# Kernel tuning notes

Hardware: AMD Instinct MI355X
Metric: run time of the kernel (lower is better)

The kernel has to match this reference:

```python
import jax, jax.numpy as jnp
import numpy as np

N = 100000   # nodes
E = 1600000  # edges (avg degree 16)
IN = 64
HID = 16     # hardcoded in ChebNet.conv1
OUT = 40
K = 3


def setup_inputs() -> dict:
    key = jax.random.key(0)
    k0, k1, k2, k3 = jax.random.split(key, 4)
    x = jax.random.normal(k0, (N, IN), jnp.float32)
    edge_index = jax.random.randint(k1, (2, E), 0, N, jnp.int32)
    # Glorot-style init for the K per-order linear maps of each ChebConv
    s1 = float(np.sqrt(2.0 / (IN + HID)))
    W1 = jax.random.normal(k2, (K, IN, HID), jnp.float32) * s1
    b1 = jnp.zeros((HID,), jnp.float32)
    s2 = float(np.sqrt(2.0 / (HID + OUT)))
    W2 = jax.random.normal(k3, (K, HID, OUT), jnp.float32) * s2
    b2 = jnp.zeros((OUT,), jnp.float32)
    return {"x": x, "edge_index": edge_index, "W1": W1, "b1": b1, "W2": W2, "b2": b2}


def cheb_conv(x, edge_index, W, b):
    """PyG ChebConv with normalization='sym', lambda_max=2.
    Scaled Laplacian: L_hat = 2L/lambda_max - I = -D^{-1/2} A D^{-1/2} (diag 0).
    out = sum_k T_k(L_hat) x @ W[k] + b, T0=x, T1=L_hat x, Tk=2 L_hat T_{k-1}-T_{k-2}.
    """
    row, col = edge_index[0], edge_index[1]
    ones = jnp.ones((edge_index.shape[1],), x.dtype)
    deg = jax.ops.segment_sum(ones, row, num_segments=N)
    dis = jnp.where(deg > 0, jax.lax.rsqrt(jnp.maximum(deg, 1.0)), 0.0)
    norm = -(dis[row] * dis[col])  # [E]

    def Lhat(z):  # sparse scatter-gather: gather src rows, scale, scatter-add to dst
        return jax.ops.segment_sum(norm[:, None] * z[row], col, num_segments=N)

    Tx0 = x
    out = Tx0 @ W[0]
    Tx1 = Lhat(x)
    if W.shape[0] > 1:
        out = out + Tx1 @ W[1]
    for k in range(2, W.shape[0]):
        Tx2 = 2.0 * Lhat(Tx1) - Tx0
        out = out + Tx2 @ W[k]
        Tx0, Tx1 = Tx1, Tx2
    return out + b


def reference(x, edge_index, W1, b1, W2, b2):
    h = jax.nn.relu(cheb_conv(x, edge_index, W1, b1))
    h = cheb_conv(h, edge_index, W2, b2)
    return jax.nn.log_softmax(h, axis=1)
```

## Files before the change

kernel.cpp:

```cpp
#include <hip/hip_runtime.h>
#include <hip/hip_bf16.h>


typedef unsigned short u16;

constexpr int N_    = 100000;
constexpr int E_    = 1600000;
constexpr int IN_   = 64;
constexpr int HID_  = 16;
constexpr int OUT_  = 40;
constexpr int CAP_  = 48;
constexpr int S_    = 64;
constexpr int EPS_  = E_ / S_;
constexpr int P8_   = 8;
constexpr int NPP8_ = N_ / P8_;
constexpr int P4_   = 4;
constexpr int NPP4_ = N_ / P4_;
constexpr int NPAD_ = 100352;

__device__ __forceinline__ float bf2f(u16 u) {
    return __uint_as_float((unsigned)u << 16);
}
__device__ __forceinline__ u16 f2bf(float x) {
    unsigned u = __float_as_uint(x);
    return (u16)((u + 0x7FFFu + ((u >> 16) & 1u)) >> 16);
}

__global__ void deg_part(const int* __restrict__ row, u16* __restrict__ partial) {
    __shared__ int lds[NPP8_];
    int p = blockIdx.x >> 6, s = blockIdx.x & 63;
    for (int i = threadIdx.x; i < NPP8_; i += 256) lds[i] = 0;
    __syncthreads();
    int lo = p * NPP8_, e0 = s * EPS_;
    for (int i = threadIdx.x; i < EPS_; i += 256) {
        int r = row[e0 + i];
        unsigned d = (unsigned)(r - lo);
        if (d < (unsigned)NPP8_) atomicAdd(&lds[d], 1);
    }
    __syncthreads();
    u16* dst = partial + (size_t)blockIdx.x * NPP8_;
    for (int i = threadIdx.x; i < NPP8_; i += 256) dst[i] = (u16)lds[i];
}

__global__ void __launch_bounds__(1024)
hist_in(const int* __restrict__ col, u16* __restrict__ partial) {
    __shared__ int lds[NPP4_];
    int p = blockIdx.x >> 6, s = blockIdx.x & 63;
    for (int i = threadIdx.x; i < NPP4_; i += 1024) lds[i] = 0;
    __syncthreads();
    int lo = p * NPP4_, e0 = s * EPS_;
    for (int i = threadIdx.x; i < EPS_; i += 1024) {
        int c = col[e0 + i];
        unsigned d = (unsigned)(c - lo);
        if (d < (unsigned)NPP4_) atomicAdd(&lds[d], 1);
    }
    __syncthreads();
    u16* dst = partial + (size_t)blockIdx.x * NPP4_;
    for (int i = threadIdx.x; i < NPP4_; i += 1024) dst[i] = (u16)lds[i];
}

__global__ void __launch_bounds__(1024)
reduce_all(const u16* __restrict__ partial_row, const u16* __restrict__ partial_in,
           float* __restrict__ dis, u16* __restrict__ pre, int* __restrict__ indeg) {
    int n = blockIdx.x * 1024 + threadIdx.x;
    if (n >= N_) return;
    {
        int p = n / NPP8_, i = n - p * NPP8_;
        const u16* base = partial_row + (size_t)(p * S_) * NPP8_ + i;
        int d = 0;
#pragma unroll 8
        for (int s = 0; s < S_; ++s) d += base[(size_t)s * NPP8_];
        dis[n] = (d > 0) ? rsqrtf((float)d) : 0.0f;
    }
    {
        int p = n / NPP4_, i = n - p * NPP4_;
        const u16* base = partial_in + (size_t)(p * S_) * NPP4_ + i;
        int run = 0;
#pragma unroll 8
        for (int s = 0; s < S_; ++s) {
            pre[(size_t)s * NPAD_ + n] = (u16)run;
            run += base[(size_t)s * NPP4_];
        }
        indeg[n] = run;
    }
}

__global__ void __launch_bounds__(1024)
place_proj(const int* __restrict__ row, const int* __restrict__ col,
           const float* __restrict__ x, const float* __restrict__ W,
           const float* __restrict__ dis, const u16* __restrict__ pre,
           int* __restrict__ bucket,
           float* __restrict__ P0f, float* __restrict__ P2f,
           u16* __restrict__ A1, u16* __restrict__ A2) {
    __shared__ int pos[NPP4_];
    __shared__ float w[3 * IN_ * HID_];
    if (blockIdx.x < 256) {
        int p = blockIdx.x >> 6, s = blockIdx.x & 63;
        int lo = p * NPP4_, e0 = s * EPS_;
        const u16* psrc = pre + (size_t)s * NPAD_ + lo;
        for (int i = threadIdx.x; i < NPP4_; i += 1024) pos[i] = psrc[i];
        __syncthreads();
        for (int i = threadIdx.x; i < EPS_; i += 1024) {
            int c = col[e0 + i];
            unsigned d = (unsigned)(c - lo);
            if (d < (unsigned)NPP4_) {
                int r = row[e0 + i];
                int q = atomicAdd(&pos[d], 1);
                if (q < CAP_) bucket[(size_t)c * CAP_ + q] = r;
            }
        }
    } else {
        for (int i = threadIdx.x; i < 3 * IN_ * HID_; i += 1024) w[i] = W[i];
        __syncthreads();
        int t = (blockIdx.x - 256) * 1024 + threadIdx.x;
        if (t >= N_ * HID_) return;
        int n = t >> 4, j = t & 15;
        const float* xr = x + (size_t)n * IN_;
        float a0 = 0.f, a1 = 0.f, a2 = 0.f;
#pragma unroll
        for (int i = 0; i < IN_; ++i) {
            float xv = xr[i];
            a0 += xv * w[i * 16 + j];
            a1 += xv * w[1024 + i * 16 + j];
            a2 += xv * w[2048 + i * 16 + j];
        }
        float dn = dis[n];
        P0f[t] = a0;
        P2f[t] = a2;
        A1[t] = f2bf(dn * a1);
        A2[t] = f2bf(dn * a2);
    }
}

__global__ void g32b(const u16* __restrict__ A1, const u16* __restrict__ A2,
                     const int* __restrict__ indeg, const int* __restrict__ bucket,
                     const float* __restrict__ dis,
                     float* __restrict__ LP1f, u16* __restrict__ B2) {
    int wib = threadIdx.x >> 6, lane = threadIdx.x & 63;
    int n0 = (blockIdx.x * 4 + wib) * 4;
    int eg = lane >> 3, sub = lane & 7;
    const u16* Z = (sub < 4) ? A1 : A2;
    int fq = sub & 3;
    int m[4];
#pragma unroll
    for (int k = 0; k < 4; ++k) m[k] = min(indeg[n0 + k], CAP_);
    float ax[4] = {0,0,0,0}, ay[4] = {0,0,0,0}, az[4] = {0,0,0,0}, aw[4] = {0,0,0,0};
#pragma unroll
    for (int k = 0; k < 4; ++k) {
        int n = n0 + k;
        for (int base = 0; base < m[k]; base += 8) {
            int e = base + eg;
            if (e < m[k]) {
                int r = bucket[n * CAP_ + e];
                ushort4 zv = *(const ushort4*)&Z[(size_t)r * 16 + fq * 4];
                ax[k] += bf2f(zv.x); ay[k] += bf2f(zv.y);
                az[k] += bf2f(zv.z); aw[k] += bf2f(zv.w);
            }
        }
    }
#pragma unroll
    for (int off = 8; off < 64; off <<= 1) {
#pragma unroll
        for (int k = 0; k < 4; ++k) {
            ax[k] += __shfl_xor(ax[k], off, 64); ay[k] += __shfl_xor(ay[k], off, 64);
            az[k] += __shfl_xor(az[k], off, 64); aw[k] += __shfl_xor(aw[k], off, 64);
        }
    }
    if (lane < 8) {
#pragma unroll
        for (int k = 0; k < 4; ++k) {
            int n = n0 + k;
            float dn = dis[n];
            if (lane < 4) {
                float4 v = {-dn * ax[k], -dn * ay[k], -dn * az[k], -dn * aw[k]};
                *(float4*)&LP1f[(size_t)n * 16 + fq * 4] = v;
            } else {
                float s = -(dn * dn);
                ushort4 v = {f2bf(s * ax[k]), f2bf(s * ay[k]),
                             f2bf(s * az[k]), f2bf(s * aw[k])};
                *(ushort4*)&B2[(size_t)n * 16 + fq * 4] = v;
            }
        }
    }
}

__device__ __forceinline__ void g16core4(const u16* __restrict__ Z,
                                         const int* __restrict__ indeg,
                                         const int* __restrict__ bucket,
                                         int n0, int lane, float4 acc[4]) {
    int eg = lane >> 2, fq = lane & 3;
    int m[4];
#pragma unroll
    for (int k = 0; k < 4; ++k) m[k] = min(indeg[n0 + k], CAP_);
    float ax[4] = {0,0,0,0}, ay[4] = {0,0,0,0}, az[4] = {0,0,0,0}, aw[4] = {0,0,0,0};
#pragma unroll
    for (int k = 0; k < 4; ++k) {
        int n = n0 + k;
        for (int base = 0; base < m[k]; base += 16) {
            int e = base + eg;
            if (e < m[k]) {
                int r = bucket[n * CAP_ + e];
                ushort4 zv = *(const ushort4*)&Z[(size_t)r * 16 + fq * 4];
                ax[k] += bf2f(zv.x); ay[k] += bf2f(zv.y);
                az[k] += bf2f(zv.z); aw[k] += bf2f(zv.w);
            }
        }
    }
#pragma unroll
    for (int off = 4; off < 64; off <<= 1) {
#pragma unroll
        for (int k = 0; k < 4; ++k) {
            ax[k] += __shfl_xor(ax[k], off, 64); ay[k] += __shfl_xor(ay[k], off, 64);
            az[k] += __shfl_xor(az[k], off, 64); aw[k] += __shfl_xor(aw[k], off, 64);
        }
    }
#pragma unroll
    for (int k = 0; k < 4; ++k) {
        float4 r4 = {ax[k], ay[k], az[k], aw[k]};
        acc[k] = r4;
    }
}

__global__ void g16_combine(const u16* __restrict__ B2, const int* __restrict__ indeg,
                            const int* __restrict__ bucket, const float* __restrict__ dis,
                            const float* __restrict__ LP1f, const float* __restrict__ P2f,
                            const float* __restrict__ b1,
                            float* p0h , u16* __restrict__ Hs) {
    int wib = threadIdx.x >> 6, lane = threadIdx.x & 63;
    int n0 = (blockIdx.x * 4 + wib) * 4;
    float4 acc[4];
    g16core4(B2, indeg, bucket, n0, lane, acc);
    if (lane < 4) {
#pragma unroll
        for (int k = 0; k < 4; ++k) {
            int n = n0 + k;
            float dn = dis[n];
            float4 p0 = *(const float4*)&p0h[(size_t)n * 16 + lane * 4];
            float4 lp = *(const float4*)&LP1f[(size_t)n * 16 + lane * 4];
            float4 p2 = *(const float4*)&P2f[(size_t)n * 16 + lane * 4];
            float4 bb = *(const float4*)&b1[lane * 4];
            float4 hv;
            hv.x = fmaxf(p0.x + lp.x - 2.f * dn * acc[k].x - p2.x + bb.x, 0.f);
            hv.y = fmaxf(p0.y + lp.y - 2.f * dn * acc[k].y - p2.y + bb.y, 0.f);
            hv.z = fmaxf(p0.z + lp.z - 2.f * dn * acc[k].z - p2.z + bb.z, 0.f);
            hv.w = fmaxf(p0.w + lp.w - 2.f * dn * acc[k].w - p2.w + bb.w, 0.f);
            *(float4*)&p0h[(size_t)n * 16 + lane * 4] = hv;
            ushort4 hs = {f2bf(dn * hv.x), f2bf(dn * hv.y),
                          f2bf(dn * hv.z), f2bf(dn * hv.w)};
            *(ushort4*)&Hs[(size_t)n * 16 + lane * 4] = hs;
        }
    }
}

__global__ void g16_t1(const u16* __restrict__ Hs, const int* __restrict__ indeg,
                       const int* __restrict__ bucket, const float* __restrict__ dis,
                       float* __restrict__ T1f, u16* __restrict__ Ts) {
    int wib = threadIdx.x >> 6, lane = threadIdx.x & 63;
    int n0 = (blockIdx.x * 4 + wib) * 4;
    float4 acc[4];
    g16core4(Hs, indeg, bucket, n0, lane, acc);
    if (lane < 4) {
#pragma unroll
        for (int k = 0; k < 4; ++k) {
            int n = n0 + k;
            float dn = dis[n];
            float4 t1 = {-dn * acc[k].x, -dn * acc[k].y, -dn * acc[k].z, -dn * acc[k].w};
            *(float4*)&T1f[(size_t)n * 16 + lane * 4] = t1;
            ushort4 ts = {f2bf(dn * t1.x), f2bf(dn * t1.y),
                          f2bf(dn * t1.z), f2bf(dn * t1.w)};
            *(ushort4*)&Ts[(size_t)n * 16 + lane * 4] = ts;
        }
    }
}

__global__ void g16_t2(const u16* __restrict__ Ts, const int* __restrict__ indeg,
                       const int* __restrict__ bucket, const float* __restrict__ dis,
                       const float* __restrict__ Hf, float* __restrict__ T2f) {
    int wib = threadIdx.x >> 6, lane = threadIdx.x & 63;
    int n0 = (blockIdx.x * 4 + wib) * 4;
    float4 acc[4];
    g16core4(Ts, indeg, bucket, n0, lane, acc);
    if (lane < 4) {
#pragma unroll
        for (int k = 0; k < 4; ++k) {
            int n = n0 + k;
            float dn = dis[n];
            float4 h4 = *(const float4*)&Hf[(size_t)n * 16 + lane * 4];
            float4 t2;
            t2.x = -2.f * dn * acc[k].x - h4.x;
            t2.y = -2.f * dn * acc[k].y - h4.y;
            t2.z = -2.f * dn * acc[k].z - h4.z;
            t2.w = -2.f * dn * acc[k].w - h4.w;
            *(float4*)&T2f[(size_t)n * 16 + lane * 4] = t2;
        }
    }
}

__global__ void __launch_bounds__(256)
mm2_lsm(const float* __restrict__ Hf, const float* __restrict__ T1f,
        const float* __restrict__ T2f, const float* __restrict__ W2,
        const float* __restrict__ b2, float* __restrict__ out) {
    int n = blockIdx.x * 256 + threadIdx.x;
    if (n >= N_) return;
    float act[48];
#pragma unroll
    for (int q = 0; q < 4; ++q)
        *(float4*)&act[q * 4] = *(const float4*)&Hf[(size_t)n * 16 + q * 4];
#pragma unroll
    for (int q = 0; q < 4; ++q)
        *(float4*)&act[16 + q * 4] = *(const float4*)&T1f[(size_t)n * 16 + q * 4];
#pragma unroll
    for (int q = 0; q < 4; ++q)
        *(float4*)&act[32 + q * 4] = *(const float4*)&T2f[(size_t)n * 16 + q * 4];
    float acc[OUT_];
#pragma unroll
    for (int o = 0; o < OUT_; ++o) acc[o] = b2[o];
#pragma unroll
    for (int j = 0; j < HID_; ++j) {
        float a0 = act[j], a1 = act[16 + j], a2 = act[32 + j];
#pragma unroll
        for (int o = 0; o < OUT_; ++o) {
            acc[o] += a0 * W2[j * OUT_ + o]
                    + a1 * W2[640 + j * OUT_ + o]
                    + a2 * W2[1280 + j * OUT_ + o];
        }
    }
    float mx = acc[0];
#pragma unroll
    for (int o = 1; o < OUT_; ++o) mx = fmaxf(mx, acc[o]);
    float s = 0.f;
#pragma unroll
    for (int o = 0; o < OUT_; ++o) s += __expf(acc[o] - mx);
    float ls = mx + logf(s);
#pragma unroll
    for (int q = 0; q < 10; ++q) {
        float4 v = {acc[q * 4] - ls, acc[q * 4 + 1] - ls,
                    acc[q * 4 + 2] - ls, acc[q * 4 + 3] - ls};
        *(float4*)&out[(size_t)n * OUT_ + q * 4] = v;
    }
}


extern "C" void kernel_launch(void* const* d_in, const int* in_sizes, int n_in,
                              void* d_out, int out_size, void* d_ws, size_t ws_size,
                              hipStream_t stream) {
    const float* x  = (const float*)d_in[0];
    const int*   ei = (const int*)d_in[1];
    const float* W1 = (const float*)d_in[2];
    const float* b1 = (const float*)d_in[3];
    const float* W2 = (const float*)d_in[4];
    const float* b2 = (const float*)d_in[5];
    float* out = (float*)d_out;

    const int* row = ei;
    const int* col = ei + E_;

    char* wp = (char*)d_ws;
    float* dis    = (float*)wp;  wp += 401408;
    int*   indeg  = (int*)wp;    wp += 401408;
    int*   bucket = (int*)wp;    wp += (size_t)N_ * CAP_ * 4;
    u16*   pre    = (u16*)wp;    wp += (size_t)S_ * NPAD_ * 2;
    char*  region = wp;
    u16* partial_row = (u16*)region;
    u16* partial_in  = (u16*)(region + 12800000);
    wp = region;
    u16*   A1   = (u16*)wp;   wp += 3211264;
    u16*   A2   = (u16*)wp;   wp += 3211264;
    u16*   B2   = (u16*)wp;   wp += 3211264;
    float* P0f  = (float*)wp; wp += 6422528;
    float* P2f  = (float*)wp; wp += 6422528;
    float* LP1f = (float*)wp; wp += 6422528;

    float* Hf  = P0f;
    u16*   Hs  = A1;
    float* T1f = LP1f;
    u16*   Ts  = A2;
    float* T2f = P2f;

    deg_part<<<P8_ * S_, 256, 0, stream>>>(row, partial_row);
    hist_in<<<P4_ * S_, 1024, 0, stream>>>(col, partial_in);
    reduce_all<<<NPAD_ / 1024, 1024, 0, stream>>>(partial_row, partial_in,
                                                  dis, pre, indeg);
    place_proj<<<256 + 1563, 1024, 0, stream>>>(row, col, x, W1, dis, pre,
                                                bucket, P0f, P2f, A1, A2);

    g32b<<<N_ / 16, 256, 0, stream>>>(A1, A2, indeg, bucket, dis, LP1f, B2);
    g16_combine<<<N_ / 16, 256, 0, stream>>>(B2, indeg, bucket, dis, LP1f, P2f, b1,
                                             P0f , Hs);
    g16_t1<<<N_ / 16, 256, 0, stream>>>(Hs, indeg, bucket, dis, T1f, Ts);
    g16_t2<<<N_ / 16, 256, 0, stream>>>(Ts, indeg, bucket, dis, Hf, T2f);
    mm2_lsm<<<(N_ + 255) / 256, 256, 0, stream>>>(Hf, T1f, T2f, W2, b2, out);
}
```

Before: 353.7 us.

## Merge row/col histogram kernels and batch bucket gathers across four nodes

The separate out-degree and in-degree histogram kernels become one launch, with blocks of both kinds in a single grid. Block indexing now interleaves partitions and edge slices so adjacent blocks read the same edge chunk. The neighbor-gather loops in g32b and g16core4 now run to the largest of the four nodes' degrees, issuing all four bucket and feature loads per iteration with a 0/1 mask instead of branching per node. This raises memory-level parallelism and saves a launch, at the cost of wasted masked loads of row 0 when degrees differ.

Measured after the change: 313.7 us. -11.3%, faster.

```diff
diff --git a/kernel.cpp b/kernel.cpp
--- a/kernel.cpp
+++ b/kernel.cpp
@@ -12,10 +12,10 @@
 constexpr int CAP_  = 48;
 constexpr int S_    = 64;
 constexpr int EPS_  = E_ / S_;
+constexpr int P4_   = 4;
+constexpr int NPP4_ = N_ / P4_;
 constexpr int P8_   = 8;
 constexpr int NPP8_ = N_ / P8_;
-constexpr int P4_   = 4;
-constexpr int NPP4_ = N_ / P4_;
 constexpr int NPAD_ = 100352;
 
 __device__ __forceinline__ float bf2f(u16 u) {
@@ -26,47 +26,48 @@
     return (u16)((u + 0x7FFFu + ((u >> 16) & 1u)) >> 16);
 }
 
-__global__ void deg_part(const int* __restrict__ row, u16* __restrict__ partial) {
-    __shared__ int lds[NPP8_];
-    int p = blockIdx.x >> 6, s = blockIdx.x & 63;
-    for (int i = threadIdx.x; i < NPP8_; i += 256) lds[i] = 0;
-    __syncthreads();
-    int lo = p * NPP8_, e0 = s * EPS_;
-    for (int i = threadIdx.x; i < EPS_; i += 256) {
-        int r = row[e0 + i];
-        unsigned d = (unsigned)(r - lo);
-        if (d < (unsigned)NPP8_) atomicAdd(&lds[d], 1);
-    }
-    __syncthreads();
-    u16* dst = partial + (size_t)blockIdx.x * NPP8_;
-    for (int i = threadIdx.x; i < NPP8_; i += 256) dst[i] = (u16)lds[i];
-}
-
 __global__ void __launch_bounds__(1024)
-hist_in(const int* __restrict__ col, u16* __restrict__ partial) {
+hist2(const int* __restrict__ row, const int* __restrict__ col,
+      u16* __restrict__ prow, u16* __restrict__ pcol) {
     __shared__ int lds[NPP4_];
-    int p = blockIdx.x >> 6, s = blockIdx.x & 63;
-    for (int i = threadIdx.x; i < NPP4_; i += 1024) lds[i] = 0;
-    __syncthreads();
-    int lo = p * NPP4_, e0 = s * EPS_;
-    for (int i = threadIdx.x; i < EPS_; i += 1024) {
-        int c = col[e0 + i];
-        unsigned d = (unsigned)(c - lo);
-        if (d < (unsigned)NPP4_) atomicAdd(&lds[d], 1);
-    }
-    __syncthreads();
-    u16* dst = partial + (size_t)blockIdx.x * NPP4_;
-    for (int i = threadIdx.x; i < NPP4_; i += 1024) dst[i] = (u16)lds[i];
+    if (blockIdx.x < P4_ * S_) {
+        int p = blockIdx.x & 3, s = blockIdx.x >> 2;
+        for (int i = threadIdx.x; i < NPP4_; i += 1024) lds[i] = 0;
+        __syncthreads();
+        int lo = p * NPP4_, e0 = s * EPS_;
+        for (int i = threadIdx.x; i < EPS_; i += 1024) {
+            int c = col[e0 + i];
+            unsigned d = (unsigned)(c - lo);
+            if (d < (unsigned)NPP4_) atomicAdd(&lds[d], 1);
+        }
+        __syncthreads();
+        u16* dst = pcol + (size_t)(p * S_ + s) * NPP4_;
+        for (int i = threadIdx.x; i < NPP4_; i += 1024) dst[i] = (u16)lds[i];
+    } else {
+        int b = blockIdx.x - P4_ * S_;
+        int p = b & 7, s = b >> 3;
+        for (int i = threadIdx.x; i < NPP8_; i += 1024) lds[i] = 0;
+        __syncthreads();
+        int lo = p * NPP8_, e0 = s * EPS_;
+        for (int i = threadIdx.x; i < EPS_; i += 1024) {
+            int r = row[e0 + i];
+            unsigned d = (unsigned)(r - lo);
+            if (d < (unsigned)NPP8_) atomicAdd(&lds[d], 1);
+        }
+        __syncthreads();
+        u16* dst = prow + (size_t)(p * S_ + s) * NPP8_;
+        for (int i = threadIdx.x; i < NPP8_; i += 1024) dst[i] = (u16)lds[i];
+    }
 }
 
 __global__ void __launch_bounds__(1024)
-reduce_all(const u16* __restrict__ partial_row, const u16* __restrict__ partial_in,
+reduce_all(const u16* __restrict__ prow, const u16* __restrict__ pcol,
            float* __restrict__ dis, u16* __restrict__ pre, int* __restrict__ indeg) {
     int n = blockIdx.x * 1024 + threadIdx.x;
     if (n >= N_) return;
     {
         int p = n / NPP8_, i = n - p * NPP8_;
-        const u16* base = partial_row + (size_t)(p * S_) * NPP8_ + i;
+        const u16* base = prow + (size_t)(p * S_) * NPP8_ + i;
         int d = 0;
 #pragma unroll 8
         for (int s = 0; s < S_; ++s) d += base[(size_t)s * NPP8_];
@@ -74,7 +75,7 @@
     }
     {
         int p = n / NPP4_, i = n - p * NPP4_;
-        const u16* base = partial_in + (size_t)(p * S_) * NPP4_ + i;
+        const u16* base = pcol + (size_t)(p * S_) * NPP4_ + i;
         int run = 0;
 #pragma unroll 8
         for (int s = 0; s < S_; ++s) {
@@ -94,8 +95,8 @@
            u16* __restrict__ A1, u16* __restrict__ A2) {
     __shared__ int pos[NPP4_];
     __shared__ float w[3 * IN_ * HID_];
-    if (blockIdx.x < 256) {
-        int p = blockIdx.x >> 6, s = blockIdx.x & 63;
+    if (blockIdx.x < P4_ * S_) {
+        int p = blockIdx.x & 3, s = blockIdx.x >> 2;
         int lo = p * NPP4_, e0 = s * EPS_;
         const u16* psrc = pre + (size_t)s * NPAD_ + lo;
         for (int i = threadIdx.x; i < NPP4_; i += 1024) pos[i] = psrc[i];
@@ -112,7 +113,7 @@
     } else {
         for (int i = threadIdx.x; i < 3 * IN_ * HID_; i += 1024) w[i] = W[i];
         __syncthreads();
-        int t = (blockIdx.x - 256) * 1024 + threadIdx.x;
+        int t = (blockIdx.x - P4_ * S_) * 1024 + threadIdx.x;
         if (t >= N_ * HID_) return;
         int n = t >> 4, j = t & 15;
         const float* xr = x + (size_t)n * IN_;
@@ -141,21 +142,25 @@
     int eg = lane >> 3, sub = lane & 7;
     const u16* Z = (sub < 4) ? A1 : A2;
     int fq = sub & 3;
-    int m[4];
-#pragma unroll
-    for (int k = 0; k < 4; ++k) m[k] = min(indeg[n0 + k], CAP_);
+    int4 mi = *(const int4*)&indeg[n0];
+    int m[4] = {min(mi.x, CAP_), min(mi.y, CAP_), min(mi.z, CAP_), min(mi.w, CAP_)};
+    int mmax = max(max(m[0], m[1]), max(m[2], m[3]));
     float ax[4] = {0,0,0,0}, ay[4] = {0,0,0,0}, az[4] = {0,0,0,0}, aw[4] = {0,0,0,0};
-#pragma unroll
-    for (int k = 0; k < 4; ++k) {
-        int n = n0 + k;
-        for (int base = 0; base < m[k]; base += 8) {
-            int e = base + eg;
-            if (e < m[k]) {
-                int r = bucket[n * CAP_ + e];
-                ushort4 zv = *(const ushort4*)&Z[(size_t)r * 16 + fq * 4];
-                ax[k] += bf2f(zv.x); ay[k] += bf2f(zv.y);
-                az[k] += bf2f(zv.z); aw[k] += bf2f(zv.w);
-            }
+    for (int base = 0; base < mmax; base += 8) {
+        int e = base + eg;
+        int rr[4]; float vm[4];
+#pragma unroll
+        for (int k = 0; k < 4; ++k) {
+            bool v = e < m[k];
+            rr[k] = bucket[(size_t)(n0 + k) * CAP_ + (v ? e : 0)];
+            vm[k] = v ? 1.0f : 0.0f;
+        }
+#pragma unroll
+        for (int k = 0; k < 4; ++k) {
+            int r = (vm[k] != 0.0f) ? rr[k] : 0;
+            ushort4 zv = *(const ushort4*)&Z[(size_t)r * 16 + fq * 4];
+            ax[k] += vm[k] * bf2f(zv.x); ay[k] += vm[k] * bf2f(zv.y);
+            az[k] += vm[k] * bf2f(zv.z); aw[k] += vm[k] * bf2f(zv.w);
         }
     }
 #pragma unroll
@@ -189,21 +194,25 @@
                                          const int* __restrict__ bucket,
                                          int n0, int lane, float4 acc[4]) {
     int eg = lane >> 2, fq = lane & 3;
-    int m[4];
-#pragma unroll
-    for (int k = 0; k < 4; ++k) m[k] = min(indeg[n0 + k], CAP_);
+    int4 mi = *(const int4*)&indeg[n0];
+    int m[4] = {min(mi.x, CAP_), min(mi.y, CAP_), min(mi.z, CAP_), min(mi.w, CAP_)};
+    int mmax = max(max(m[0], m[1]), max(m[2], m[3]));
     float ax[4] = {0,0,0,0}, ay[4] = {0,0,0,0}, az[4] = {0,0,0,0}, aw[4] = {0,0,0,0};
-#pragma unroll
-    for (int k = 0; k < 4; ++k) {
-        int n = n0 + k;
-        for (int base = 0; base < m[k]; base += 16) {
-            int e = base + eg;
-            if (e < m[k]) {
-                int r = bucket[n * CAP_ + e];
-                ushort4 zv = *(const ushort4*)&Z[(size_t)r * 16 + fq * 4];
-                ax[k] += bf2f(zv.x); ay[k] += bf2f(zv.y);
-                az[k] += bf2f(zv.z); aw[k] += bf2f(zv.w);
-            }
+    for (int base = 0; base < mmax; base += 16) {
+        int e = base + eg;
+        int rr[4]; float vm[4];
+#pragma unroll
+        for (int k = 0; k < 4; ++k) {
+            bool v = e < m[k];
+            rr[k] = bucket[(size_t)(n0 + k) * CAP_ + (v ? e : 0)];
+            vm[k] = v ? 1.0f : 0.0f;
+        }
+#pragma unroll
+        for (int k = 0; k < 4; ++k) {
+            int r = (vm[k] != 0.0f) ? rr[k] : 0;
+            ushort4 zv = *(const ushort4*)&Z[(size_t)r * 16 + fq * 4];
+            ax[k] += vm[k] * bf2f(zv.x); ay[k] += vm[k] * bf2f(zv.y);
+            az[k] += vm[k] * bf2f(zv.z); aw[k] += vm[k] * bf2f(zv.w);
         }
     }
 #pragma unroll
@@ -361,8 +370,8 @@
     int*   bucket = (int*)wp;    wp += (size_t)N_ * CAP_ * 4;
     u16*   pre    = (u16*)wp;    wp += (size_t)S_ * NPAD_ * 2;
     char*  region = wp;
-    u16* partial_row = (u16*)region;
-    u16* partial_in  = (u16*)(region + 12800000);
+    u16* pcol = (u16*)region;
+    u16* prow = (u16*)(region + 12800000);
     wp = region;
     u16*   A1   = (u16*)wp;   wp += 3211264;
     u16*   A2   = (u16*)wp;   wp += 3211264;
@@ -377,12 +386,10 @@
     u16*   Ts  = A2;
     float* T2f = P2f;
 
-    deg_part<<<P8_ * S_, 256, 0, stream>>>(row, partial_row);
-    hist_in<<<P4_ * S_, 1024, 0, stream>>>(col, partial_in);
-    reduce_all<<<NPAD_ / 1024, 1024, 0, stream>>>(partial_row, partial_in,
-                                                  dis, pre, indeg);
-    place_proj<<<256 + 1563, 1024, 0, stream>>>(row, col, x, W1, dis, pre,
-                                                bucket, P0f, P2f, A1, A2);
+    hist2<<<P4_ * S_ + P8_ * S_, 1024, 0, stream>>>(row, col, prow, pcol);
+    reduce_all<<<NPAD_ / 1024, 1024, 0, stream>>>(prow, pcol, dis, pre, indeg);
+    place_proj<<<P4_ * S_ + 1563, 1024, 0, stream>>>(row, col, x, W1, dis, pre,
+                                                     bucket, P0f, P2f, A1, A2);
 
     g32b<<<N_ / 16, 256, 0, stream>>>(A1, A2, indeg, bucket, dis, LP1f, B2);
     g16_combine<<<N_ / 16, 256, 0, stream>>>(B2, indeg, bucket, dis, LP1f, P2f, b1,
```
